# Kernel optimization log

Measured on AMD Instinct MI355X. Metric: run time of the kernel, lower is better.

The kernel has to match this reference:

```python
import jax, jax.numpy as jnp
import numpy as np

H, N, CH = 256, 64, 1

def _r2c(x):
    return x[..., 0] + 1j * x[..., 1]

def setup_inputs() -> dict:
    key = jax.random.key(0)
    kA, kB, kC, kdt = jax.random.split(key, 4)
    # Build a Hurwitz A (skew-Hermitian - 0.5*I) so dA = (I-dt/2 A)^-1 (I+dt/2 A) has spectral radius < 1
    M = jax.random.normal(kA, (H, N, N, 2), dtype=jnp.float32) / np.float32(np.sqrt(N))
    Mc = _r2c(M)
    Ac = 0.5 * (Mc - jnp.conjugate(jnp.swapaxes(Mc, -1, -2))) - 0.5 * jnp.eye(N, dtype=Mc.dtype)
    A = jnp.stack([Ac.real, Ac.imag], axis=-1)  # (H,N,N,2)
    B = jax.random.normal(kB, (H, N, 2), dtype=jnp.float32)
    C = jax.random.normal(kC, (CH, H, N, 2), dtype=jnp.float32)
    # log_dt uniform in [log(1e-3), log(1e-1)], shape (H,1) per bilinear docstring
    log_dt = jax.random.uniform(kdt, (H, 1), dtype=jnp.float32,
                                minval=np.float32(np.log(1e-3)), maxval=np.float32(np.log(1e-1)))
    return {"A": A, "B": B, "C": C, "log_dt": log_dt, "L": 2048}

def _bilinear(dt, Ac, Bc):
    # dt: (H,1), Ac: (H,N,N) complex, Bc: (H,N) complex
    n = Ac.shape[-1]
    I = jnp.eye(n, dtype=Ac.dtype)
    half = (dt.astype(Ac.real.dtype) / 2)[:, None]  # (H,1,1)
    A_back = I - half * Ac
    A_fwd = I + half * Ac
    dB = dt.astype(Ac.dtype) * jnp.linalg.solve(A_back, Bc[..., None])[..., 0]  # (H,N)
    dA = jnp.linalg.solve(A_back, A_fwd)  # (H,N,N)
    return dA, dB

def _krylov(L, dA, dB):
    # x[..., l] = dA^l dB via squaring-doubling, matches S4 krylov math
    x = dB[..., None]  # (H,N,1)
    A_ = dA
    while x.shape[-1] < L:
        x = jnp.concatenate([x, jnp.einsum('hnm,hml->hnl', A_, x)], axis=-1)
        A_ = A_ @ A_
    return x[..., :L]

def reference(A, B, C, log_dt, L):
    Ac, Bc, Cc = _r2c(A), _r2c(B), _r2c(C)
    dt = jnp.exp(log_dt)  # (H,1)
    dA, dB = _bilinear(dt, Ac, Bc)
    x = _krylov(L, dA, dB)  # (H,N,L) complex
    # k[c,h,l] = sum_n C[c,h,n] * (dA^l dB)[h,n]; torch .float() on complex keeps real part
    k = jnp.einsum('chn,hnl->chl', Cc, x).real.astype(jnp.float32)
    return k
```

## Files before the change

### kernel.cpp

```cpp
#include <hip/hip_runtime.h>
#include <math.h>

#define NH   256
#define NN   64
#define LSEQ 2048
#define SDW  68
#define NTH  1024

typedef __attribute__((ext_vector_type(8))) short short8;
typedef __attribute__((ext_vector_type(4))) float float4_t;

#define MFMA(a,b,c) __builtin_amdgcn_mfma_f32_16x16x32_bf16((a),(b),(c),0,0,0)
#define PERM_HI 0x07060302u
#define PERM_LO 0x05040100u

static __device__ __forceinline__ unsigned pack2(float v) {
    unsigned hv = __float_as_uint(v) & 0xffff0000u;
    float lo = v - __uint_as_float(hv);
    return __builtin_amdgcn_perm(hv, __float_as_uint(lo), PERM_HI);
}
static __device__ __forceinline__ float unpack2(unsigned w) {
    return __uint_as_float(w & 0xffff0000u) + __uint_as_float(w << 16);
}

static __device__ __forceinline__ void frag_vals(const unsigned* e, short8& hi, short8& lo) {
    unsigned lb[8];
#pragma unroll
    for (int m = 0; m < 8; ++m) {
        unsigned hv = e[m] & 0xffff0000u;
        lb[m] = __float_as_uint(__uint_as_float(e[m]) - __uint_as_float(hv));
    }
    union { short8 s; unsigned u[4]; } H, L;
#pragma unroll
    for (int m = 0; m < 4; ++m) {
        H.u[m] = __builtin_amdgcn_perm(e[2*m+1],  e[2*m],  PERM_HI);
        L.u[m] = __builtin_amdgcn_perm(lb[2*m+1], lb[2*m], PERM_HI);
    }
    hi = H.s; lo = L.s;
}
static __device__ __forceinline__ void frag_f32(const float* p, short8& hi, short8& lo) {
    const uint4* q = (const uint4*)p;
    uint4 d0 = q[0], d1 = q[1];
    unsigned e[8] = {d0.x, d0.y, d0.z, d0.w, d1.x, d1.y, d1.z, d1.w};
    frag_vals(e, hi, lo);
}
static __device__ __forceinline__ void frag_packed(const unsigned* p, short8& hi, short8& lo) {
    const uint4* q = (const uint4*)p;
    uint4 d0 = q[0], d1 = q[1];
    unsigned e[8] = {d0.x, d0.y, d0.z, d0.w, d1.x, d1.y, d1.z, d1.w};
    union { short8 s; unsigned u[4]; } H, L;
#pragma unroll
    for (int m = 0; m < 4; ++m) {
        H.u[m] = __builtin_amdgcn_perm(e[2*m+1], e[2*m], PERM_HI);
        L.u[m] = __builtin_amdgcn_perm(e[2*m+1], e[2*m], PERM_LO);
    }
    hi = H.s; lo = L.s;
}
static __device__ __forceinline__ short8 neg8(short8 v) {
    union { short8 s; int i[4]; } u; u.s = v;
#pragma unroll
    for (int m = 0; m < 4; ++m) u.i[m] ^= 0x80008000;
    return u.s;
}

template<bool AP, bool BP, bool IMAG>
static __device__ __forceinline__ void cmm_tile(
    const void* Ar_, const void* Ai_, const void* Br_, const void* Bi_,
    int arow, int bcol, int fq, float4_t& accR, float4_t& accI)
{
#pragma unroll
    for (int ks = 0; ks < 2; ++ks) {
        const int k0 = ks*32 + fq*8;
        short8 Arh, Arl, Aih, Ail, Brh, Brl, Bih, Bil;
        if (AP) {
            frag_packed((const unsigned*)Ar_ + arow*SDW + k0, Arh, Arl);
            frag_packed((const unsigned*)Ai_ + arow*SDW + k0, Aih, Ail);
        } else {
            frag_f32((const float*)Ar_ + arow*SDW + k0, Arh, Arl);
            frag_f32((const float*)Ai_ + arow*SDW + k0, Aih, Ail);
        }
        if (BP) {
            frag_packed((const unsigned*)Br_ + bcol*SDW + k0, Brh, Brl);
            frag_packed((const unsigned*)Bi_ + bcol*SDW + k0, Bih, Bil);
        } else {
            frag_f32((const float*)Br_ + bcol*SDW + k0, Brh, Brl);
            frag_f32((const float*)Bi_ + bcol*SDW + k0, Bih, Bil);
        }
        short8 nAih = neg8(Aih), nAil = neg8(Ail);
        accR = MFMA(Arh, Brh, accR); accR = MFMA(Arh, Brl, accR); accR = MFMA(Arl, Brh, accR);
        accR = MFMA(nAih, Bih, accR); accR = MFMA(nAih, Bil, accR); accR = MFMA(nAil, Bih, accR);
        if (IMAG) {
            accI = MFMA(Arh, Bih, accI); accI = MFMA(Arh, Bil, accI); accI = MFMA(Arl, Bih, accI);
            accI = MFMA(Aih, Brh, accI); accI = MFMA(Aih, Brl, accI); accI = MFMA(Ail, Brh, accI);
        }
    }
}

__global__ __launch_bounds__(NTH, 4) void ssm_kernel(
    const float* __restrict__ Ag,
    const float* __restrict__ Bg,
    const float* __restrict__ Cg,
    const float* __restrict__ LogDt,
    float* __restrict__ outp)
{
    __shared__ __align__(16) unsigned char lds[130688];
    unsigned* XRr = (unsigned*)(lds +      0);
    unsigned* XRi = (unsigned*)(lds +  17408);
    unsigned* XTr = (unsigned*)(lds +  34816);
    unsigned* XTi = (unsigned*)(lds +  52224);
    float*    Xfr = (float*)(lds +  69632);
    float*    Xfi = (float*)(lds +  87040);
    unsigned* U0u = (unsigned*)Xfr;
    unsigned* U1u = (unsigned*)Xfi;
    float*    Grf = (float*)(lds + 104448);
    float*    Gif = (float*)(lds + 113152);
    float*    Kof = (float*)(lds + 121856);
    float*    bvr = (float*)(lds + 130176);
    float*    bvi = (float*)(lds + 130432);

    const int t    = threadIdx.x;
    const int lane = t & 63;
    const int wv   = t >> 6;
    const int ti   = wv >> 2, tj = wv & 3;
    const int fm   = lane & 15, fq = lane >> 4;
    const int h    = blockIdx.x;

    const float dt  = expf(LogDt[h]);
    const float hdt = 0.5f * dt;

    const float2* A2 = (const float2*)(Ag + (size_t)h * NN * NN * 2);
    const float4_t z4 = {0.f, 0.f, 0.f, 0.f};

#pragma unroll
    for (int e = 0; e < 4; ++e) {
        int idx = t + e*NTH;
        int i = idx >> 6, j = idx & 63;
        float2 a = A2[idx];
        unsigned pr = pack2((i == j ? 1.0f : 0.0f) + hdt * a.x);
        unsigned pi = pack2(hdt * a.y);
        XRr[i*SDW + j] = pr; XRi[i*SDW + j] = pi;
        XTr[j*SDW + i] = pr; XTi[j*SDW + i] = pi;
    }
    if (t < NN) {
        float2 bv = ((const float2*)Bg)[h*NN + t];
        float2 cv = ((const float2*)Cg)[h*NN + t];
        bvr[t] = bv.x; bvi[t] = bv.y;
        Grf[t] = cv.x; Gif[t] = cv.y;
    }
    __syncthreads();

    const int arow = ti*16 + fm;
    const int bcol = tj*16 + fm;

    {
        float4_t aR = z4, aI = z4;
#pragma unroll
        for (int ks = 0; ks < 2; ++ks) {
            const int k0 = ks*32 + fq*8;
            unsigned vr[8], vi[8];
#pragma unroll
            for (int j = 0; j < 8; ++j) {
                float2 a = A2[arow*NN + k0 + j];
                vr[j] = __float_as_uint((arow == k0 + j ? 1.0f : 0.0f) - hdt * a.x);
                vi[j] = __float_as_uint(-hdt * a.y);
            }
            short8 Arh, Arl, Aih, Ail, Brh, Brl, Bih, Bil;
            frag_vals(vr, Arh, Arl);
            frag_vals(vi, Aih, Ail);
            frag_packed(XTr + bcol*SDW + k0, Brh, Brl);
            frag_packed(XTi + bcol*SDW + k0, Bih, Bil);
            short8 nAih = neg8(Aih), nAil = neg8(Ail);
            aR = MFMA(Arh, Brh, aR); aR = MFMA(Arh, Brl, aR); aR = MFMA(Arl, Brh, aR);
            aR = MFMA(nAih, Bih, aR); aR = MFMA(nAih, Bil, aR); aR = MFMA(nAil, Bih, aR);
            aI = MFMA(Arh, Bih, aI); aI = MFMA(Arh, Bil, aI); aI = MFMA(Arl, Bih, aI);
            aI = MFMA(Aih, Brh, aI); aI = MFMA(Aih, Brl, aI); aI = MFMA(Ail, Brh, aI);
        }
#pragma unroll
        for (int rp = 0; rp < 2; ++rp) {
            int row0 = ti*16 + fq*4 + rp*2;
            uint2 wr; wr.x = pack2(aR[rp*2]); wr.y = pack2(aR[rp*2+1]);
            uint2 wi; wi.x = pack2(aI[rp*2]); wi.y = pack2(aI[rp*2+1]);
            *(uint2*)(U0u + bcol*SDW + row0) = wr;
            *(uint2*)(U1u + bcol*SDW + row0) = wi;
        }
    }
    __syncthreads();

    {
        float4_t aR = z4, aI = z4;
        cmm_tile<true, true, true>(XRr, XRi, U0u, U1u, arow, bcol, fq, aR, aI);
        __syncthreads();
#pragma unroll
        for (int r = 0; r < 4; ++r) {
            int row = ti*16 + fq*4 + r;
            XRr[row*SDW + bcol] = pack2(aR[r]);
            XRi[row*SDW + bcol] = pack2(aI[r]);
        }
    }
    __syncthreads();

    {
        float4_t aR = z4, aI = z4;
        cmm_tile<true, true, true>(XRr, XRi, U0u, U1u, arow, bcol, fq, aR, aI);
        float o_r[4], o_i[4];
#pragma unroll
        for (int r = 0; r < 4; ++r) {
            int row = ti*16 + fq*4 + r;
            float2 a = A2[row*NN + bcol];
            float x1r = (row == bcol ? 1.0f : 0.0f) + hdt * a.x;
            float x1i = hdt * a.y;
            float vvr = unpack2(XRr[row*SDW + bcol]);
            float vvi = unpack2(XRi[row*SDW + bcol]);
            o_r[r] = 3.0f*x1r - 3.0f*vvr + aR[r];
            o_i[r] = 3.0f*x1i - 3.0f*vvi + aI[r];
        }
        __syncthreads();
        unsigned pr[4], pi[4];
#pragma unroll
        for (int r = 0; r < 4; ++r) {
            int row = ti*16 + fq*4 + r;
            pr[r] = pack2(o_r[r]); pi[r] = pack2(o_i[r]);
            XRr[row*SDW + bcol] = pr[r]; XRi[row*SDW + bcol] = pi[r];
        }
#pragma unroll
        for (int rp = 0; rp < 2; ++rp) {
            int row0 = ti*16 + fq*4 + rp*2;
            uint2 wr; wr.x = pr[rp*2]; wr.y = pr[rp*2+1];
            uint2 wi; wi.x = pi[rp*2]; wi.y = pi[rp*2+1];
            *(uint2*)(XTr + bcol*SDW + row0) = wr;
            *(uint2*)(XTi + bcol*SDW + row0) = wi;
        }
    }
    __syncthreads();

    {
        int n = t >> 4, part = t & 15;
        float ar = 0.f, ai = 0.f;
#pragma unroll
        for (int qq = 0; qq < 4; ++qq) {
            int k = part + 16*qq;
            float mr = unpack2(XRr[n*SDW + k]), mi = unpack2(XRi[n*SDW + k]);
            ar += mr*bvr[k] - mi*bvi[k];
            ai += mr*bvi[k] + mi*bvr[k];
        }
#pragma unroll
        for (int off = 8; off; off >>= 1) { ar += __shfl_xor(ar, off); ai += __shfl_xor(ai, off); }
        if (part == 0) { Xfr[n] = dt*ar; Xfi[n] = dt*ai; }
    }
    __syncthreads();

#pragma unroll
    for (int e = 0; e < 4; ++e) {
        int idx = t + e*NTH;
        int i = idx >> 6, j = idx & 63;
        float vr = 2.0f*unpack2(XRr[i*SDW + j]) - (i == j ? 1.0f : 0.0f);
        float vi = 2.0f*unpack2(XRi[i*SDW + j]);
        unsigned pr = pack2(vr), pi = pack2(vi);
        XRr[i*SDW + j] = pr; XRi[i*SDW + j] = pi;
        XTr[j*SDW + i] = pr; XTi[j*SDW + i] = pi;
    }
    __syncthreads();

#pragma unroll 1
    for (int s = 1; s <= 9; ++s) {
        if (s <= 6) {
            const int C = 1 << (s-1);
            const int nT = (s == 6) ? 8 : 4;
            if (wv < nT) {
                const int rt = wv >> 2, ct = wv & 3;
                float4_t aR = z4, aI = z4;
                cmm_tile<false, true, true>(Xfr, Xfi, XRr, XRi, rt*16 + fm, ct*16 + fm, fq, aR, aI);
#pragma unroll
                for (int r = 0; r < 4; ++r) {
                    int row = rt*16 + fq*4 + r;
                    Xfr[(C+row)*SDW + ct*16 + fm] = aR[r];
                    Xfi[(C+row)*SDW + ct*16 + fm] = aI[r];
                }
            }
        } else {
            const int C = 1 << (s-7);
            if (wv < 4) {
                float4_t aR = z4, aI = z4;
                cmm_tile<false, true, true>(Grf, Gif, XTr, XTi, fm, wv*16 + fm, fq, aR, aI);
#pragma unroll
                for (int r = 0; r < 4; ++r) {
                    int row = fq*4 + r;
                    Grf[(C+row)*SDW + wv*16 + fm] = aR[r];
                    Gif[(C+row)*SDW + wv*16 + fm] = aI[r];
                }
            }
        }
        float4_t sR = z4, sI = z4;
        cmm_tile<true, true, true>(XRr, XRi, XTr, XTi, arow, bcol, fq, sR, sI);
        __syncthreads();
        unsigned pr[4], pi[4];
#pragma unroll
        for (int r = 0; r < 4; ++r) {
            int row = ti*16 + fq*4 + r;
            pr[r] = pack2(sR[r]); pi[r] = pack2(sI[r]);
            XRr[row*SDW + bcol] = pr[r]; XRi[row*SDW + bcol] = pi[r];
        }
#pragma unroll
        for (int rp = 0; rp < 2; ++rp) {
            int row0 = ti*16 + fq*4 + rp*2;
            uint2 wr; wr.x = pr[rp*2]; wr.y = pr[rp*2+1];
            uint2 wi; wi.x = pi[rp*2]; wi.y = pi[rp*2+1];
            *(uint2*)(XTr + bcol*SDW + row0) = wr;
            *(uint2*)(XTi + bcol*SDW + row0) = wi;
        }
        __syncthreads();
    }

#pragma unroll 1
    for (int tt = 0; tt < 4; ++tt) {
        if (tt < 3 && wv < 4) {
            const int ab = tt * 8;
            float4_t aR = z4, aI = z4;
            cmm_tile<false, true, true>(Grf, Gif, XTr, XTi, ab + fm, wv*16 + fm, fq, aR, aI);
#pragma unroll
            for (int r = 0; r < 4; ++r) {
                int orow = 8 + ab + fq*4 + r;
                if (orow < 32) {
                    Grf[orow*SDW + wv*16 + fm] = aR[r];
                    Gif[orow*SDW + wv*16 + fm] = aI[r];
                }
            }
        }
        if (wv >= 4 && wv < 8) {
            const int jb = tt * 8;
            float4_t aR = z4, aI = z4;
            cmm_tile<false, false, false>(Grf, Gif, Xfr, Xfi, jb + fm, (wv-4)*16 + fm, fq, aR, aI);
            if (fq < 2) {
#pragma unroll
                for (int r = 0; r < 4; ++r)
                    Kof[(jb + fq*4 + r)*65 + (wv-4)*16 + fm] = aR[r];
            }
        }
        __syncthreads();
    }

    {
        int row = t >> 5, col = (t & 31) * 2;
        float2 v = { Kof[row*65 + col], Kof[row*65 + col + 1] };
        ((float2*)(outp + (size_t)h * LSEQ))[t] = v;
    }
}

extern "C" void kernel_launch(void* const* d_in, const int* in_sizes, int n_in,
                              void* d_out, int out_size, void* d_ws, size_t ws_size,
                              hipStream_t stream) {
    const float* A  = (const float*)d_in[0];
    const float* B  = (const float*)d_in[1];
    const float* C  = (const float*)d_in[2];
    const float* ld = (const float*)d_in[3];
    float* out = (float*)d_out;
    ssm_kernel<<<dim3(NH), dim3(NTH), 0, stream>>>(A, B, C, ld, out);
}
```

Before: 97.18 us.

## Store bf16 hi/lo split planes in LDS and fold dA transform into step

Result: slower. 99.78 us (+2.7%).

```diff
diff --git a/kernel.cpp b/kernel.cpp
--- a/kernel.cpp
+++ b/kernel.cpp
@@ -4,25 +4,28 @@
 #define NH   256
 #define NN   64
 #define LSEQ 2048
-#define SDW  68
+#define SB   72
 #define NTH  1024
 
 typedef __attribute__((ext_vector_type(8))) short short8;
 typedef __attribute__((ext_vector_type(4))) float float4_t;
+typedef unsigned short u16;
 
 #define MFMA(a,b,c) __builtin_amdgcn_mfma_f32_16x16x32_bf16((a),(b),(c),0,0,0)
 #define PERM_HI 0x07060302u
-#define PERM_LO 0x05040100u
-
-static __device__ __forceinline__ unsigned pack2(float v) {
-    unsigned hv = __float_as_uint(v) & 0xffff0000u;
-    float lo = v - __uint_as_float(hv);
-    return __builtin_amdgcn_perm(hv, __float_as_uint(lo), PERM_HI);
-}
-static __device__ __forceinline__ float unpack2(unsigned w) {
-    return __uint_as_float(w & 0xffff0000u) + __uint_as_float(w << 16);
-}
-
+
+static __device__ __forceinline__ void split1(float v, u16& h, u16& l) {
+    unsigned u = __float_as_uint(v);
+    unsigned hv = u & 0xffff0000u;
+    h = (u16)(u >> 16);
+    l = (u16)(__float_as_uint(v - __uint_as_float(hv)) >> 16);
+}
+static __device__ __forceinline__ float join1(u16 h, u16 l) {
+    return __uint_as_float((unsigned)h << 16) + __uint_as_float((unsigned)l << 16);
+}
+static __device__ __forceinline__ void st2(u16* base, int idx, u16 a, u16 b) {
+    *(unsigned*)(base + idx) = (unsigned)a | ((unsigned)b << 16);
+}
 static __device__ __forceinline__ void frag_vals(const unsigned* e, short8& hi, short8& lo) {
     unsigned lb[8];
 #pragma unroll
@@ -38,24 +41,6 @@
     }
     hi = H.s; lo = L.s;
 }
-static __device__ __forceinline__ void frag_f32(const float* p, short8& hi, short8& lo) {
-    const uint4* q = (const uint4*)p;
-    uint4 d0 = q[0], d1 = q[1];
-    unsigned e[8] = {d0.x, d0.y, d0.z, d0.w, d1.x, d1.y, d1.z, d1.w};
-    frag_vals(e, hi, lo);
-}
-static __device__ __forceinline__ void frag_packed(const unsigned* p, short8& hi, short8& lo) {
-    const uint4* q = (const uint4*)p;
-    uint4 d0 = q[0], d1 = q[1];
-    unsigned e[8] = {d0.x, d0.y, d0.z, d0.w, d1.x, d1.y, d1.z, d1.w};
-    union { short8 s; unsigned u[4]; } H, L;
-#pragma unroll
-    for (int m = 0; m < 4; ++m) {
-        H.u[m] = __builtin_amdgcn_perm(e[2*m+1], e[2*m], PERM_HI);
-        L.u[m] = __builtin_amdgcn_perm(e[2*m+1], e[2*m], PERM_LO);
-    }
-    hi = H.s; lo = L.s;
-}
 static __device__ __forceinline__ short8 neg8(short8 v) {
     union { short8 s; int i[4]; } u; u.s = v;
 #pragma unroll
@@ -63,35 +48,30 @@
     return u.s;
 }
 
-template<bool AP, bool BP, bool IMAG>
+template<bool IMAG>
 static __device__ __forceinline__ void cmm_tile(
-    const void* Ar_, const void* Ai_, const void* Br_, const void* Bi_,
+    const u16* Arh, const u16* Arl, const u16* Aih, const u16* Ail,
+    const u16* Brh, const u16* Brl, const u16* Bih, const u16* Bil,
     int arow, int bcol, int fq, float4_t& accR, float4_t& accI)
 {
 #pragma unroll
     for (int ks = 0; ks < 2; ++ks) {
         const int k0 = ks*32 + fq*8;
-        short8 Arh, Arl, Aih, Ail, Brh, Brl, Bih, Bil;
-        if (AP) {
-            frag_packed((const unsigned*)Ar_ + arow*SDW + k0, Arh, Arl);
-            frag_packed((const unsigned*)Ai_ + arow*SDW + k0, Aih, Ail);
-        } else {
-            frag_f32((const float*)Ar_ + arow*SDW + k0, Arh, Arl);
-            frag_f32((const float*)Ai_ + arow*SDW + k0, Aih, Ail);
-        }
-        if (BP) {
-            frag_packed((const unsigned*)Br_ + bcol*SDW + k0, Brh, Brl);
-            frag_packed((const unsigned*)Bi_ + bcol*SDW + k0, Bih, Bil);
-        } else {
-            frag_f32((const float*)Br_ + bcol*SDW + k0, Brh, Brl);
-            frag_f32((const float*)Bi_ + bcol*SDW + k0, Bih, Bil);
-        }
-        short8 nAih = neg8(Aih), nAil = neg8(Ail);
-        accR = MFMA(Arh, Brh, accR); accR = MFMA(Arh, Brl, accR); accR = MFMA(Arl, Brh, accR);
-        accR = MFMA(nAih, Bih, accR); accR = MFMA(nAih, Bil, accR); accR = MFMA(nAil, Bih, accR);
+        const int ao = arow*SB + k0, bo = bcol*SB + k0;
+        short8 arh = *(const short8*)(Arh + ao);
+        short8 arl = *(const short8*)(Arl + ao);
+        short8 aih = *(const short8*)(Aih + ao);
+        short8 ail = *(const short8*)(Ail + ao);
+        short8 brh = *(const short8*)(Brh + bo);
+        short8 brl = *(const short8*)(Brl + bo);
+        short8 bih = *(const short8*)(Bih + bo);
+        short8 bil = *(const short8*)(Bil + bo);
+        short8 naih = neg8(aih), nail = neg8(ail);
+        accR = MFMA(arh, brh, accR); accR = MFMA(arh, brl, accR); accR = MFMA(arl, brh, accR);
+        accR = MFMA(naih, bih, accR); accR = MFMA(naih, bil, accR); accR = MFMA(nail, bih, accR);
         if (IMAG) {
-            accI = MFMA(Arh, Bih, accI); accI = MFMA(Arh, Bil, accI); accI = MFMA(Arl, Bih, accI);
-            accI = MFMA(Aih, Brh, accI); accI = MFMA(Aih, Brl, accI); accI = MFMA(Ail, Brh, accI);
+            accI = MFMA(arh, bih, accI); accI = MFMA(arh, bil, accI); accI = MFMA(arl, bih, accI);
+            accI = MFMA(aih, brh, accI); accI = MFMA(aih, brl, accI); accI = MFMA(ail, brh, accI);
         }
     }
 }
@@ -103,20 +83,27 @@
     const float* __restrict__ LogDt,
     float* __restrict__ outp)
 {
-    __shared__ __align__(16) unsigned char lds[130688];
-    unsigned* XRr = (unsigned*)(lds +      0);
-    unsigned* XRi = (unsigned*)(lds +  17408);
-    unsigned* XTr = (unsigned*)(lds +  34816);
-    unsigned* XTi = (unsigned*)(lds +  52224);
-    float*    Xfr = (float*)(lds +  69632);
-    float*    Xfi = (float*)(lds +  87040);
-    unsigned* U0u = (unsigned*)Xfr;
-    unsigned* U1u = (unsigned*)Xfi;
-    float*    Grf = (float*)(lds + 104448);
-    float*    Gif = (float*)(lds + 113152);
-    float*    Kof = (float*)(lds + 121856);
-    float*    bvr = (float*)(lds + 130176);
-    float*    bvi = (float*)(lds + 130432);
+    __shared__ __align__(16) unsigned char lds[130048];
+    u16* XRrh = (u16*)(lds +      0);
+    u16* XRrl = (u16*)(lds +   9216);
+    u16* XRih = (u16*)(lds +  18432);
+    u16* XRil = (u16*)(lds +  27648);
+    u16* XTrh = (u16*)(lds +  36864);
+    u16* XTrl = (u16*)(lds +  46080);
+    u16* XTih = (u16*)(lds +  55296);
+    u16* XTil = (u16*)(lds +  64512);
+    u16* Xfrh = (u16*)(lds +  73728);
+    u16* Xfrl = (u16*)(lds +  82944);
+    u16* Xfih = (u16*)(lds +  92160);
+    u16* Xfil = (u16*)(lds + 101376);
+    u16* Grh  = (u16*)(lds + 110592);
+    u16* Grl  = (u16*)(lds + 115200);
+    u16* Gih  = (u16*)(lds + 119808);
+    u16* Gil  = (u16*)(lds + 124416);
+    float* bvr = (float*)(lds + 129024);
+    float* bvi = (float*)(lds + 129280);
+    float* urr = (float*)(lds + 129536);
+    float* uri = (float*)(lds + 129792);
 
     const int t    = threadIdx.x;
     const int lane = t & 63;
@@ -136,16 +123,21 @@
         int idx = t + e*NTH;
         int i = idx >> 6, j = idx & 63;
         float2 a = A2[idx];
-        unsigned pr = pack2((i == j ? 1.0f : 0.0f) + hdt * a.x);
-        unsigned pi = pack2(hdt * a.y);
-        XRr[i*SDW + j] = pr; XRi[i*SDW + j] = pi;
-        XTr[j*SDW + i] = pr; XTi[j*SDW + i] = pi;
+        u16 rh, rl, ih, il;
+        split1((i == j ? 1.0f : 0.0f) + hdt * a.x, rh, rl);
+        split1(hdt * a.y, ih, il);
+        XRrh[i*SB + j] = rh; XRrl[i*SB + j] = rl;
+        XRih[i*SB + j] = ih; XRil[i*SB + j] = il;
+        XTrh[j*SB + i] = rh; XTrl[j*SB + i] = rl;
+        XTih[j*SB + i] = ih; XTil[j*SB + i] = il;
     }
     if (t < NN) {
         float2 bv = ((const float2*)Bg)[h*NN + t];
         float2 cv = ((const float2*)Cg)[h*NN + t];
         bvr[t] = bv.x; bvi[t] = bv.y;
-        Grf[t] = cv.x; Gif[t] = cv.y;
+        u16 hh, ll;
+        split1(cv.x, hh, ll); Grh[t] = hh; Grl[t] = ll;
+        split1(cv.y, hh, ll); Gih[t] = hh; Gil[t] = ll;
     }
     __syncthreads();
 
@@ -164,72 +156,75 @@
                 vr[j] = __float_as_uint((arow == k0 + j ? 1.0f : 0.0f) - hdt * a.x);
                 vi[j] = __float_as_uint(-hdt * a.y);
             }
-            short8 Arh, Arl, Aih, Ail, Brh, Brl, Bih, Bil;
-            frag_vals(vr, Arh, Arl);
-            frag_vals(vi, Aih, Ail);
-            frag_packed(XTr + bcol*SDW + k0, Brh, Brl);
-            frag_packed(XTi + bcol*SDW + k0, Bih, Bil);
-            short8 nAih = neg8(Aih), nAil = neg8(Ail);
-            aR = MFMA(Arh, Brh, aR); aR = MFMA(Arh, Brl, aR); aR = MFMA(Arl, Brh, aR);
-            aR = MFMA(nAih, Bih, aR); aR = MFMA(nAih, Bil, aR); aR = MFMA(nAil, Bih, aR);
-            aI = MFMA(Arh, Bih, aI); aI = MFMA(Arh, Bil, aI); aI = MFMA(Arl, Bih, aI);
-            aI = MFMA(Aih, Brh, aI); aI = MFMA(Aih, Brl, aI); aI = MFMA(Ail, Brh, aI);
-        }
-#pragma unroll
-        for (int rp = 0; rp < 2; ++rp) {
-            int row0 = ti*16 + fq*4 + rp*2;
-            uint2 wr; wr.x = pack2(aR[rp*2]); wr.y = pack2(aR[rp*2+1]);
-            uint2 wi; wi.x = pack2(aI[rp*2]); wi.y = pack2(aI[rp*2+1]);
-            *(uint2*)(U0u + bcol*SDW + row0) = wr;
-            *(uint2*)(U1u + bcol*SDW + row0) = wi;
-        }
+            short8 arh, arl, aih, ail;
+            frag_vals(vr, arh, arl);
+            frag_vals(vi, aih, ail);
+            const int bo = bcol*SB + k0;
+            short8 brh = *(const short8*)(XTrh + bo);
+            short8 brl = *(const short8*)(XTrl + bo);
+            short8 bih = *(const short8*)(XTih + bo);
+            short8 bil = *(const short8*)(XTil + bo);
+            short8 naih = neg8(aih), nail = neg8(ail);
+            aR = MFMA(arh, brh, aR); aR = MFMA(arh, brl, aR); aR = MFMA(arl, brh, aR);
+            aR = MFMA(naih, bih, aR); aR = MFMA(naih, bil, aR); aR = MFMA(nail, bih, aR);
+            aI = MFMA(arh, bih, aI); aI = MFMA(arh, bil, aI); aI = MFMA(arl, bih, aI);
+            aI = MFMA(aih, brh, aI); aI = MFMA(aih, brl, aI); aI = MFMA(ail, brh, aI);
+        }
+        u16 hr[4], lr[4], hi_[4], li_[4];
+#pragma unroll
+        for (int r = 0; r < 4; ++r) { split1(aR[r], hr[r], lr[r]); split1(aI[r], hi_[r], li_[r]); }
+        const int tb = bcol*SB + ti*16 + fq*4;
+        st2(Xfrh, tb, hr[0], hr[1]); st2(Xfrh, tb+2, hr[2], hr[3]);
+        st2(Xfrl, tb, lr[0], lr[1]); st2(Xfrl, tb+2, lr[2], lr[3]);
+        st2(Xfih, tb, hi_[0], hi_[1]); st2(Xfih, tb+2, hi_[2], hi_[3]);
+        st2(Xfil, tb, li_[0], li_[1]); st2(Xfil, tb+2, li_[2], li_[3]);
     }
     __syncthreads();
 
     {
         float4_t aR = z4, aI = z4;
-        cmm_tile<true, true, true>(XRr, XRi, U0u, U1u, arow, bcol, fq, aR, aI);
+        cmm_tile<true>(XRrh,XRrl,XRih,XRil, Xfrh,Xfrl,Xfih,Xfil, arow, bcol, fq, aR, aI);
         __syncthreads();
 #pragma unroll
         for (int r = 0; r < 4; ++r) {
             int row = ti*16 + fq*4 + r;
-            XRr[row*SDW + bcol] = pack2(aR[r]);
-            XRi[row*SDW + bcol] = pack2(aI[r]);
+            u16 hh, ll;
+            split1(aR[r], hh, ll); XRrh[row*SB + bcol] = hh; XRrl[row*SB + bcol] = ll;
+            split1(aI[r], hh, ll); XRih[row*SB + bcol] = hh; XRil[row*SB + bcol] = ll;
         }
     }
     __syncthreads();
 
     {
         float4_t aR = z4, aI = z4;
-        cmm_tile<true, true, true>(XRr, XRi, U0u, U1u, arow, bcol, fq, aR, aI);
-        float o_r[4], o_i[4];
+        cmm_tile<true>(XRrh,XRrl,XRih,XRil, Xfrh,Xfrl,Xfih,Xfil, arow, bcol, fq, aR, aI);
+        float p_r[4], p_i[4];
 #pragma unroll
         for (int r = 0; r < 4; ++r) {
             int row = ti*16 + fq*4 + r;
             float2 a = A2[row*NN + bcol];
             float x1r = (row == bcol ? 1.0f : 0.0f) + hdt * a.x;
             float x1i = hdt * a.y;
-            float vvr = unpack2(XRr[row*SDW + bcol]);
-            float vvi = unpack2(XRi[row*SDW + bcol]);
-            o_r[r] = 3.0f*x1r - 3.0f*vvr + aR[r];
-            o_i[r] = 3.0f*x1i - 3.0f*vvi + aI[r];
+            float vvr = join1(XRrh[row*SB + bcol], XRrl[row*SB + bcol]);
+            float vvi = join1(XRih[row*SB + bcol], XRil[row*SB + bcol]);
+            p_r[r] = 2.0f*(3.0f*x1r - 3.0f*vvr + aR[r]) - (row == bcol ? 1.0f : 0.0f);
+            p_i[r] = 2.0f*(3.0f*x1i - 3.0f*vvi + aI[r]);
         }
         __syncthreads();
-        unsigned pr[4], pi[4];
+        u16 hr[4], lr[4], hi_[4], li_[4];
+#pragma unroll
+        for (int r = 0; r < 4; ++r) { split1(p_r[r], hr[r], lr[r]); split1(p_i[r], hi_[r], li_[r]); }
 #pragma unroll
         for (int r = 0; r < 4; ++r) {
             int row = ti*16 + fq*4 + r;
-            pr[r] = pack2(o_r[r]); pi[r] = pack2(o_i[r]);
-            XRr[row*SDW + bcol] = pr[r]; XRi[row*SDW + bcol] = pi[r];
-        }
-#pragma unroll
-        for (int rp = 0; rp < 2; ++rp) {
-            int row0 = ti*16 + fq*4 + rp*2;
-            uint2 wr; wr.x = pr[rp*2]; wr.y = pr[rp*2+1];
-            uint2 wi; wi.x = pi[rp*2]; wi.y = pi[rp*2+1];
-            *(uint2*)(XTr + bcol*SDW + row0) = wr;
-            *(uint2*)(XTi + bcol*SDW + row0) = wi;
-        }
+            XRrh[row*SB + bcol] = hr[r]; XRrl[row*SB + bcol] = lr[r];
+            XRih[row*SB + bcol] = hi_[r]; XRil[row*SB + bcol] = li_[r];
+        }
+        const int tb = bcol*SB + ti*16 + fq*4;
+        st2(XTrh, tb, hr[0], hr[1]); st2(XTrh, tb+2, hr[2], hr[3]);
+        st2(XTrl, tb, lr[0], lr[1]); st2(XTrl, tb+2, lr[2], lr[3]);
+        st2(XTih, tb, hi_[0], hi_[1]); st2(XTih, tb+2, hi_[2], hi_[3]);
+        st2(XTil, tb, li_[0], li_[1]); st2(XTil, tb+2, li_[2], li_[3]);
     }
     __syncthreads();
 
@@ -239,75 +234,90 @@
 #pragma unroll
         for (int qq = 0; qq < 4; ++qq) {
             int k = part + 16*qq;
-            float mr = unpack2(XRr[n*SDW + k]), mi = unpack2(XRi[n*SDW + k]);
+            float mr = join1(XRrh[n*SB + k], XRrl[n*SB + k]);
+            float mi = join1(XRih[n*SB + k], XRil[n*SB + k]);
             ar += mr*bvr[k] - mi*bvi[k];
             ai += mr*bvi[k] + mi*bvr[k];
         }
 #pragma unroll
         for (int off = 8; off; off >>= 1) { ar += __shfl_xor(ar, off); ai += __shfl_xor(ai, off); }
-        if (part == 0) { Xfr[n] = dt*ar; Xfi[n] = dt*ai; }
-    }
-    __syncthreads();
-
-#pragma unroll
-    for (int e = 0; e < 4; ++e) {
-        int idx = t + e*NTH;
-        int i = idx >> 6, j = idx & 63;
-        float vr = 2.0f*unpack2(XRr[i*SDW + j]) - (i == j ? 1.0f : 0.0f);
-        float vi = 2.0f*unpack2(XRi[i*SDW + j]);
-        unsigned pr = pack2(vr), pi = pack2(vi);
-        XRr[i*SDW + j] = pr; XRi[i*SDW + j] = pi;
-        XTr[j*SDW + i] = pr; XTi[j*SDW + i] = pi;
+        if (part == 0) { urr[n] = ar; uri[n] = ai; }
     }
     __syncthreads();
 
 #pragma unroll 1
     for (int s = 1; s <= 9; ++s) {
-        if (s <= 6) {
+        if (s == 1) {
+            int n = t >> 4, part = t & 15;
+            float ar = 0.f, ai = 0.f;
+#pragma unroll
+            for (int qq = 0; qq < 4; ++qq) {
+                int k = part + 16*qq;
+                float mr = join1(XRrh[n*SB + k], XRrl[n*SB + k]);
+                float mi = join1(XRih[n*SB + k], XRil[n*SB + k]);
+                ar += mr*urr[k] - mi*uri[k];
+                ai += mr*uri[k] + mi*urr[k];
+            }
+#pragma unroll
+            for (int off = 8; off; off >>= 1) { ar += __shfl_xor(ar, off); ai += __shfl_xor(ai, off); }
+            if (part == 0) {
+                float u_r = urr[n], u_i = uri[n];
+                u16 hh, ll;
+                split1(hdt*(u_r + bvr[n]), hh, ll); Xfrh[n] = hh; Xfrl[n] = ll;
+                split1(hdt*(u_i + bvi[n]), hh, ll); Xfih[n] = hh; Xfil[n] = ll;
+                split1(hdt*(ar + u_r), hh, ll); Xfrh[SB + n] = hh; Xfrl[SB + n] = ll;
+                split1(hdt*(ai + u_i), hh, ll); Xfih[SB + n] = hh; Xfil[SB + n] = ll;
+            }
+        } else if (s <= 6) {
             const int C = 1 << (s-1);
             const int nT = (s == 6) ? 8 : 4;
             if (wv < nT) {
-                const int rt = wv >> 2, ct = wv & 3;
+                int rt = wv >> 2, ct = wv & 3;
                 float4_t aR = z4, aI = z4;
-                cmm_tile<false, true, true>(Xfr, Xfi, XRr, XRi, rt*16 + fm, ct*16 + fm, fq, aR, aI);
+                cmm_tile<true>(Xfrh,Xfrl,Xfih,Xfil, XRrh,XRrl,XRih,XRil,
+                               rt*16 + fm, ct*16 + fm, fq, aR, aI);
 #pragma unroll
                 for (int r = 0; r < 4; ++r) {
-                    int row = rt*16 + fq*4 + r;
-                    Xfr[(C+row)*SDW + ct*16 + fm] = aR[r];
-                    Xfi[(C+row)*SDW + ct*16 + fm] = aI[r];
+                    int row = C + rt*16 + fq*4 + r;
+                    int col = ct*16 + fm;
+                    u16 hh, ll;
+                    split1(aR[r], hh, ll); Xfrh[row*SB + col] = hh; Xfrl[row*SB + col] = ll;
+                    split1(aI[r], hh, ll); Xfih[row*SB + col] = hh; Xfil[row*SB + col] = ll;
                 }
             }
         } else {
             const int C = 1 << (s-7);
             if (wv < 4) {
                 float4_t aR = z4, aI = z4;
-                cmm_tile<false, true, true>(Grf, Gif, XTr, XTi, fm, wv*16 + fm, fq, aR, aI);
+                cmm_tile<true>(Grh,Grl,Gih,Gil, XTrh,XTrl,XTih,XTil,
+                               fm, wv*16 + fm, fq, aR, aI);
 #pragma unroll
                 for (int r = 0; r < 4; ++r) {
-                    int row = fq*4 + r;
-                    Grf[(C+row)*SDW + wv*16 + fm] = aR[r];
-                    Gif[(C+row)*SDW + wv*16 + fm] = aI[r];
+                    int row = C + fq*4 + r;
+                    int col = wv*16 + fm;
+                    u16 hh, ll;
+                    split1(aR[r], hh, ll); Grh[row*SB + col] = hh; Grl[row*SB + col] = ll;
+                    split1(aI[r], hh, ll); Gih[row*SB + col] = hh; Gil[row*SB + col] = ll;
                 }
             }
         }
         float4_t sR = z4, sI = z4;
-        cmm_tile<true, true, true>(XRr, XRi, XTr, XTi, arow, bcol, fq, sR, sI);
+        cmm_tile<true>(XRrh,XRrl,XRih,XRil, XTrh,XTrl,XTih,XTil, arow, bcol, fq, sR, sI);
         __syncthreads();
-        unsigned pr[4], pi[4];
+        u16 hr[4], lr[4], hi_[4], li_[4];
+#pragma unroll
+        for (int r = 0; r < 4; ++r) { split1(sR[r], hr[r], lr[r]); split1(sI[r], hi_[r], li_[r]); }
 #pragma unroll
         for (int r = 0; r < 4; ++r) {
             int row = ti*16 + fq*4 + r;
-            pr[r] = pack2(sR[r]); pi[r] = pack2(sI[r]);
-            XRr[row*SDW + bcol] = pr[r]; XRi[row*SDW + bcol] = pi[r];
-        }
-#pragma unroll
-        for (int rp = 0; rp < 2; ++rp) {
-            int row0 = ti*16 + fq*4 + rp*2;
-            uint2 wr; wr.x = pr[rp*2]; wr.y = pr[rp*2+1];
-            uint2 wi; wi.x = pi[rp*2]; wi.y = pi[rp*2+1];
-            *(uint2*)(XTr + bcol*SDW + row0) = wr;
-            *(uint2*)(XTi + bcol*SDW + row0) = wi;
-        }
+            XRrh[row*SB + bcol] = hr[r]; XRrl[row*SB + bcol] = lr[r];
+            XRih[row*SB + bcol] = hi_[r]; XRil[row*SB + bcol] = li_[r];
+        }
+        const int tb = bcol*SB + ti*16 + fq*4;
+        st2(XTrh, tb, hr[0], hr[1]); st2(XTrh, tb+2, hr[2], hr[3]);
+        st2(XTrl, tb, lr[0], lr[1]); st2(XTrl, tb+2, lr[2], lr[3]);
+        st2(XTih, tb, hi_[0], hi_[1]); st2(XTih, tb+2, hi_[2], hi_[3]);
+        st2(XTil, tb, li_[0], li_[1]); st2(XTil, tb+2, li_[2], li_[3]);
         __syncthreads();
     }
 
@@ -316,33 +326,32 @@
         if (tt < 3 && wv < 4) {
             const int ab = tt * 8;
             float4_t aR = z4, aI = z4;
-            cmm_tile<false, true, true>(Grf, Gif, XTr, XTi, ab + fm, wv*16 + fm, fq, aR, aI);
+            cmm_tile<true>(Grh,Grl,Gih,Gil, XTrh,XTrl,XTih,XTil,
+                           ab + fm, wv*16 + fm, fq, aR, aI);
 #pragma unroll
             for (int r = 0; r < 4; ++r) {
-                int orow = 8 + ab + fq*4 + r;
-                if (orow < 32) {
-                    Grf[orow*SDW + wv*16 + fm] = aR[r];
-                    Gif[orow*SDW + wv*16 + fm] = aI[r];
+                int row = 8 + ab + fq*4 + r;
+                if (row < 32) {
+                    int col = wv*16 + fm;
+                    u16 hh, ll;
+                    split1(aR[r], hh, ll); Grh[row*SB + col] = hh; Grl[row*SB + col] = ll;
+                    split1(aI[r], hh, ll); Gih[row*SB + col] = hh; Gil[row*SB + col] = ll;
                 }
             }
         }
         if (wv >= 4 && wv < 8) {
             const int jb = tt * 8;
             float4_t aR = z4, aI = z4;
-            cmm_tile<false, false, false>(Grf, Gif, Xfr, Xfi, jb + fm, (wv-4)*16 + fm, fq, aR, aI);
+            cmm_tile<false>(Grh,Grl,Gih,Gil, Xfrh,Xfrl,Xfih,Xfil,
+                            jb + fm, (wv-4)*16 + fm, fq, aR, aI);
             if (fq < 2) {
+                size_t base = (size_t)h * LSEQ;
 #pragma unroll
                 for (int r = 0; r < 4; ++r)
-                    Kof[(jb + fq*4 + r)*65 + (wv-4)*16 + fm] = aR[r];
-            }
-        }
-        __syncthreads();
-    }
-
-    {
-        int row = t >> 5, col = (t & 31) * 2;
-        float2 v = { Kof[row*65 + col], Kof[row*65 + col + 1] };
-        ((float2*)(outp + (size_t)h * LSEQ))[t] = v;
+                    outp[base + (jb + fq*4 + r)*NN + (wv-4)*16 + fm] = aR[r];
+            }
+        }
+        if (tt < 3) __syncthreads();
     }
 }
 
```
